# Performance work log

Measured on AMD Instinct MI355X. Metric: run time of the kernel, lower is better.

The kernel has to match this reference:

```python
import jax, jax.numpy as jnp
import numpy as np

B, C, H, W = 32, 512, 28, 28
NUM_CLASSES = 200
THRESHOLD = 0.6


def _conv(x, w, b, pad):
    y = jax.lax.conv_general_dilated(
        x, w, window_strides=(1, 1), padding=[(pad, pad), (pad, pad)],
        dimension_numbers=('NCHW', 'OIHW', 'NCHW'))
    return y + b[None, :, None, None]


def _classifier(x, w1, b1, w2, b2, w3, b3):
    x = jax.nn.relu(_conv(x, w1, b1, 1))
    x = jax.nn.relu(_conv(x, w2, b2, 1))
    return _conv(x, w3, b3, 0)


def _avg_pool3(x):
    # torch F.avg_pool2d(k=3, stride=1, pad=1, count_include_pad=True): sum window / 9
    s = jax.lax.reduce_window(x, 0.0, jax.lax.add, (1, 1, 3, 3), (1, 1, 1, 1),
                              [(0, 0), (0, 0), (1, 1), (1, 1)])
    return s / 9.0


def setup_inputs() -> dict:
    key = jax.random.key(0)
    ks = jax.random.split(key, 16)
    sc = 0.02
    inp = {
        'x': jax.random.normal(ks[0], (B, C, H, W), jnp.float32),
        'label': jax.random.randint(ks[1], (B, NUM_CLASSES), 0, 2),
        'w1a': jax.random.normal(ks[2], (1024, 512, 3, 3), jnp.float32) * sc,
        'b1a': jax.random.normal(ks[3], (1024,), jnp.float32) * sc,
        'w2a': jax.random.normal(ks[4], (1024, 1024, 3, 3), jnp.float32) * sc,
        'b2a': jax.random.normal(ks[5], (1024,), jnp.float32) * sc,
        'w3a': jax.random.normal(ks[6], (NUM_CLASSES, 1024, 1, 1), jnp.float32) * sc,
        'b3a': jax.random.normal(ks[7], (NUM_CLASSES,), jnp.float32) * sc,
        'w1b': jax.random.normal(ks[8], (1024, 512, 3, 3), jnp.float32) * sc,
        'b1b': jax.random.normal(ks[9], (1024,), jnp.float32) * sc,
        'w2b': jax.random.normal(ks[10], (1024, 1024, 3, 3), jnp.float32) * sc,
        'b2b': jax.random.normal(ks[11], (1024,), jnp.float32) * sc,
        'w3b': jax.random.normal(ks[12], (NUM_CLASSES, 1024, 1, 1), jnp.float32) * sc,
        'b3b': jax.random.normal(ks[13], (NUM_CLASSES,), jnp.float32) * sc,
    }
    return inp


def reference(x, label, w1a, b1a, w2a, b2a, w3a, b3a,
              w1b, b1b, w2b, b2b, w3b, b3b):
    feats = _avg_pool3(x)                       # [B,512,H,W]
    out_A = _classifier(feats, w1a, b1a, w2a, b2a, w3a, b3a)  # [B,K,H,W]
    logits_A = out_A.mean(axis=(2, 3))          # [B,K]

    # attention map: per-sample max over channels whose label is nonzero,
    # floored at 0 (the loop seeds the channel stack with a zeros map)
    sel = jnp.where(label[:, :, None, None] > 0, out_A, -jnp.inf)
    atten = jnp.maximum(sel.max(axis=1), 0.0)   # [B,H,W]

    # per-sample min-max normalization over HxW
    mins = atten.min(axis=(1, 2), keepdims=True)
    maxs = atten.max(axis=(1, 2), keepdims=True)
    atten_n = (atten - mins) / (maxs - mins)

    # threshold-erase mask (constant w.r.t. autograd, matching torch code)
    mask = jax.lax.stop_gradient(jnp.where(atten_n >= THRESHOLD, 0.0, 1.0))
    feats_erased = feats * mask[:, None, :, :]

    out_B = _classifier(feats_erased, w1b, b1b, w2b, b2b, w3b, b3b)
    logits_B = out_B.mean(axis=(2, 3))
    return logits_A, logits_B
```

## Files before the change

kernel.cpp:

```cpp
#include <hip/hip_runtime.h>
#include <hip/hip_bf16.h>

typedef unsigned long long ull;
typedef __attribute__((ext_vector_type(8))) short short8;
typedef __attribute__((ext_vector_type(8))) __bf16 bf16x8;
typedef __attribute__((ext_vector_type(4))) float floatx4;

#define GLL16(gp, lp) __builtin_amdgcn_global_load_lds( \
  (__attribute__((address_space(1))) void*)(gp), \
  (__attribute__((address_space(3))) void*)(lp), 16, 0, 0)

#define WVM(N) asm volatile("s_waitcnt vmcnt(" #N ")" ::: "memory")

__device__ __forceinline__ floatx4 mfma16(short8 a, short8 b, floatx4 c){
  return __builtin_amdgcn_mfma_f32_16x16x32_bf16(
      __builtin_bit_cast(bf16x8, a), __builtin_bit_cast(bf16x8, b), c, 0, 0, 0);
}

__device__ __forceinline__ unsigned pkbf(float a, float b){
  unsigned ua = __float_as_uint(a), ub = __float_as_uint(b);
  ua += 0x7fffu + ((ua >> 16) & 1u);
  ub += 0x7fffu + ((ub >> 16) & 1u);
  return (ua >> 16) | (ub & 0xffff0000u);
}

__global__ __launch_bounds__(256) void pool_kernel(const float* __restrict__ x,
                                                   unsigned short* __restrict__ out){
  __shared__ float xs[16*784];
  const int tid = threadIdx.x;
  const int b = blockIdx.x >> 5, cg = blockIdx.x & 31;
  const float* src = x + ((size_t)b*512 + cg*16)*784;
  for (int i=tid;i<16*784;i+=256) xs[i]=src[i];
  __syncthreads();
  unsigned* dst = (unsigned*)out + ((size_t)b*960)*256 + cg*8;
  for (int o=tid;o<30*32*8;o+=256){
    int cip = o & 7, pos = o >> 3;
    int row = pos >> 5, col = pos & 31;
    float s0=0.f, s1=0.f;
    if (row>=1 && row<=28 && col>=1 && col<=28){
      int h=row-1, w=col-1;
      const float* p0 = &xs[(cip*2)*784];
      const float* p1 = p0 + 784;
      #pragma unroll
      for (int dh=-1;dh<=1;++dh){ int hh=h+dh; if ((unsigned)hh<28u){
        #pragma unroll
        for (int dw=-1;dw<=1;++dw){ int ww=w+dw; if((unsigned)ww<28u){
          s0 += p0[hh*28+ww]; s1 += p1[hh*28+ww]; } } } }
      s0 /= 9.f; s1 /= 9.f;
    }
    dst[(size_t)pos*256 + cip] = pkbf(s0, s1);
  }
}

template<int CIN>
__global__ __launch_bounds__(256) void prep3x3(const float* __restrict__ w,
                                               unsigned short* __restrict__ Wt){
  __shared__ float wsm[CIN*9];
  const int co = blockIdx.x, tid = threadIdx.x;
  const float* src = w + (size_t)co*(CIN*9);
  for (int i=tid;i<CIN*9;i+=256) wsm[i]=src[i];
  __syncthreads();
  for (int o=tid;o<9*(CIN/2);o+=256){
    int t = o/(CIN/2), cp = o - t*(CIN/2);
    unsigned v = pkbf(wsm[(cp*2)*9+t], wsm[(cp*2+1)*9+t]);
    ((unsigned*)Wt)[(((size_t)t*1024+co)*CIN>>1) + cp] = v;
  }
}

__global__ __launch_bounds__(256) void prep1x1(const float* __restrict__ w3,
                                               unsigned short* __restrict__ Wp){
  const int row = blockIdx.x, tid = threadIdx.x;
  unsigned* dst = (unsigned*)Wp + (size_t)row*512;
  if (row < 200){
    const float* src = w3 + (size_t)row*1024;
    for (int j=tid;j<512;j+=256) dst[j] = pkbf(src[2*j], src[2*j+1]);
  } else {
    for (int j=tid;j<512;j+=256) dst[j] = 0u;
  }
}

template<int CIN>
__global__ __launch_bounds__(256, 2) void conv3x3_v10(
    const unsigned short* __restrict__ X,
    const unsigned short* __restrict__ Wt,
    const float* __restrict__ bias,
    unsigned short* __restrict__ Out)
{
  constexpr int NCH = CIN/32;
  constexpr size_t CB = (size_t)CIN*2;
  constexpr size_t TAPSTR = (size_t)1024*CB;
  __shared__ char Als[24576];
  __shared__ char Bls[20480];

  const int tid = threadIdx.x;
  const int l = tid & 63, wv = tid >> 6;
  const int cog = wv & 1, pg = wv >> 1;
  const int bid = blockIdx.x;
  const int co0 = (bid & 7) << 7;
  const int y = bid >> 3;
  const int b = y >> 2, rb = y & 3;
  const int r0 = rb << 3;
  const bool active = (pg == 0) || (rb < 3);

  const int sbyt = (l*16) ^ (((l>>3)&7)<<4);
  const int srow = sbyt >> 6;
  const int sw   = sbyt & 63;

  const ull aS0 = (ull)Wt + (size_t)(co0 + (wv*2)*16   + srow)*CB + sw;
  const ull aS1 = (ull)Wt + (size_t)(co0 + (wv*2+1)*16 + srow)*CB + sw;
  ull bS[5];
  #pragma unroll
  for (int k=0;k<5;++k){
    int q = (wv + 4*k)*16 + srow;
    int trow = q >> 5, tcol = q & 31;
    int ir = r0 + trow; if (ir > 29) ir = 29;
    bS[k] = (ull)X + ((size_t)b*960 + ir*32 + tcol)*CB + sw;
  }

  const int jl = l & 15, g = l >> 4;
  int paE[4];
  #pragma unroll
  for (int m=0;m<4;++m){
    int xo = (cog*64 + m*16 + jl)*64 + g*16;
    paE[m] = xo ^ (((xo>>7)&7)<<4);
  }
  int pbS[3][7];
  #pragma unroll
  for (int f=0;f<7;++f){
    int p = pg*112 + f*16 + jl;
    int hl = p/28, cl = p - hl*28;
    #pragma unroll
    for (int ss=0;ss<3;++ss){
      int xo = (hl*32 + cl + ss)*64 + g*16;
      pbS[ss][f] = xo ^ (((xo>>7)&7)<<4);
    }
  }

  floatx4 acc[4][7];
  #pragma unroll
  for (int m=0;m<4;++m)
    #pragma unroll
    for (int f=0;f<7;++f) acc[m][f] = (floatx4){0.f,0.f,0.f,0.f};

  #pragma unroll
  for (int k=0;k<5;++k) GLL16((const void*)bS[k], Bls + (wv + 4*k)*1024);
  GLL16((const void*)aS0,            Als +        (wv*2)*1024);
  GLL16((const void*)aS1,            Als +        (wv*2+1)*1024);
  GLL16((const void*)(aS0 + TAPSTR), Als + 8192 + (wv*2)*1024);
  GLL16((const void*)(aS1 + TAPSTR), Als + 8192 + (wv*2+1)*1024);

  #pragma unroll 1
  for (int c=0;c<NCH;++c){
    #pragma unroll
    for (int t=0;t<9;++t){
      const int rr = t/3, ss = t - rr*3;
      if (t == 0 && c > 0){
        #pragma unroll
        for (int k=0;k<5;++k)
          GLL16((const void*)(bS[k] + (size_t)c*64), Bls + (wv + 4*k)*1024);
      }
      {
        const int stTap = (t<7) ? t+2 : t-7;
        const size_t aoff = (size_t)stTap*TAPSTR + (size_t)(c + (t>=7))*64;
        const int sd = ((t+2)%3)*8192;
        GLL16((const void*)(aS0 + aoff), Als + sd + (wv*2)*1024);
        GLL16((const void*)(aS1 + aoff), Als + sd + (wv*2+1)*1024);
      }
      if (t == 0) { WVM(2); } else { WVM(4); }
      __builtin_amdgcn_s_barrier();
      if (active){
        const char* ap = Als + (t%3)*8192;
        short8 a0 = *(const short8*)(ap + paE[0]);
        short8 a1 = *(const short8*)(ap + paE[1]);
        short8 a2 = *(const short8*)(ap + paE[2]);
        short8 a3 = *(const short8*)(ap + paE[3]);
        short8 bv[7];
        #pragma unroll
        for (int f=0;f<7;++f)
          bv[f] = *(const short8*)(Bls + (pbS[ss][f] + rr*2048));
        __builtin_amdgcn_s_setprio(1);
        #pragma unroll
        for (int f=0;f<7;++f){
          acc[0][f] = mfma16(a0, bv[f], acc[0][f]);
          acc[1][f] = mfma16(a1, bv[f], acc[1][f]);
          acc[2][f] = mfma16(a2, bv[f], acc[2][f]);
          acc[3][f] = mfma16(a3, bv[f], acc[3][f]);
        }
        __builtin_amdgcn_s_setprio(0);
      }
      __builtin_amdgcn_s_barrier();
    }
  }

  if (!active) return;

  #pragma unroll
  for (int m=0;m<4;++m){
    const int coL = cog*64 + m*16 + g*4;
    const float4 bv4 = *(const float4*)&bias[co0 + coL];
    #pragma unroll
    for (int f=0;f<7;++f){
      int pp = pg*112 + f*16 + jl;
      int hl = pp/28, cl = pp - hl*28;
      float v0 = fmaxf(acc[m][f][0] + bv4.x, 0.f);
      float v1 = fmaxf(acc[m][f][1] + bv4.y, 0.f);
      float v2 = fmaxf(acc[m][f][2] + bv4.z, 0.f);
      float v3 = fmaxf(acc[m][f][3] + bv4.w, 0.f);
      uint2 pk; pk.x = pkbf(v0,v1); pk.y = pkbf(v2,v3);
      size_t oa = ((size_t)b*960 + (size_t)(r0 + hl + 1)*32 + (cl + 1))*1024 + (co0 + coL);
      *(uint2*)(Out + oa) = pk;
    }
  }
}

template<int CIN, bool K3, bool BF16OUT>
__global__ __launch_bounds__(512, 2) void conv_mfma(
    const unsigned short* __restrict__ X,
    const unsigned short* __restrict__ Wt,
    const float* __restrict__ bias, int biasN,
    void* __restrict__ Out)
{
  constexpr int T9 = K3 ? 9 : 1;
  constexpr int NA = K3 ? 9 : 1;
  __shared__ short Als[T9*4096];
  __shared__ short Bls[10240];
  __shared__ float biasLs[128];

  const int tid = threadIdx.x;
  const int l = tid & 63, wv = tid >> 6;
  const int wc = wv & 3, wp = wv >> 2;
  const int co0 = blockIdx.x << 7;
  const int by = blockIdx.y;
  const int b = by >> 2, rb = by & 3;
  const int r0 = rb << 3;
  const int nrh = (rb < 3) ? 10 : 6;
  const int NB = 2*nrh;
  const bool active = (wp == 0) || (rb < 3);

  if (tid < 128) biasLs[tid] = (co0 + tid < biasN) ? bias[co0 + tid] : 0.f;

  const size_t laneOff = (size_t)(l >> 2)*(CIN*2) + (size_t)(l & 3)*16;

  ull aB[NA];
  #pragma unroll
  for (int j=0;j<NA;++j){
    int k = wv*NA + j;
    int t = K3 ? (k >> 3) : 0;
    int cog2 = K3 ? (k & 7) : k;
    aB[j] = (ull)Wt + ((size_t)(t*1024 + co0 + cog2*16)*(CIN*2)) + laneOff;
  }
  const ull xBase = (ull)X + ((size_t)b*960)*(CIN*2) + (size_t)(r0*32)*(CIN*2) + laneOff;
  ull bB0=0, bB1=0, bB2=0; int nb=0;
  if (wv < NB)      { bB0 = xBase + (size_t)(wv*16)*(CIN*2);      nb = 1; }
  if (wv + 8 < NB)  { bB1 = xBase + (size_t)((wv+8)*16)*(CIN*2);  nb = 2; }
  if (wv + 16 < NB) { bB2 = xBase + (size_t)((wv+16)*16)*(CIN*2); nb = 3; }

  const int jl = l & 15, g = l >> 4;
  int paE[2];
  #pragma unroll
  for (int m=0;m<2;++m) paE[m] = (wc*32 + m*16 + jl)*32 + g*8;
  int pbE[7], ph[7], pc[7];
  #pragma unroll
  for (int f=0;f<7;++f){
    int p = wp*112 + f*16 + jl;
    int hl = p / 28, cl = p - hl*28;
    ph[f]=hl; pc[f]=cl;
    pbE[f] = (hl*32 + cl)*32 + g*8;
  }

  floatx4 acc[2][7];
  #pragma unroll
  for (int m=0;m<2;++m)
    #pragma unroll
    for (int f=0;f<7;++f) acc[m][f] = (floatx4){0.f,0.f,0.f,0.f};

  const int NCH = CIN/32;
  for (int c=0;c<NCH;++c){
    if (c) __syncthreads();
    const size_t cOff = (size_t)c*64;
    #pragma unroll
    for (int j=0;j<NA;++j)
      GLL16((const void*)(aB[j] + cOff), (char*)Als + (wv*NA + j)*1024);
    GLL16((const void*)(bB0 + cOff), (char*)Bls + wv*1024);
    if (nb > 1) GLL16((const void*)(bB1 + cOff), (char*)Bls + (wv+8)*1024);
    if (nb > 2) GLL16((const void*)(bB2 + cOff), (char*)Bls + (wv+16)*1024);
    __syncthreads();
    if (active){
      #pragma unroll
      for (int t=0;t<T9;++t){
        const int tA = t*4096;
        const int tB = K3 ? (((t/3)*32 + (t - (t/3)*3))*32) : ((1*32+1)*32);
        short8 a0 = *(const short8*)&Als[tA + paE[0]];
        short8 a1 = *(const short8*)&Als[tA + paE[1]];
        #pragma unroll
        for (int f=0;f<7;++f){
          short8 bvv = *(const short8*)&Bls[tB + pbE[f]];
          acc[0][f] = mfma16(a0, bvv, acc[0][f]);
          acc[1][f] = mfma16(a1, bvv, acc[1][f]);
        }
      }
    }
  }

  if (!active) return;

  #pragma unroll
  for (int m=0;m<2;++m){
    const int coL = wc*32 + m*16 + g*4;
    const float4 bv4 = *(const float4*)&biasLs[coL];
    #pragma unroll
    for (int f=0;f<7;++f){
      float v0 = acc[m][f][0] + bv4.x;
      float v1 = acc[m][f][1] + bv4.y;
      float v2 = acc[m][f][2] + bv4.z;
      float v3 = acc[m][f][3] + bv4.w;
      if constexpr (BF16OUT){
        v0=fmaxf(v0,0.f); v1=fmaxf(v1,0.f); v2=fmaxf(v2,0.f); v3=fmaxf(v3,0.f);
        uint2 pk; pk.x = pkbf(v0,v1); pk.y = pkbf(v2,v3);
        size_t oa = ((size_t)b*960 + (size_t)(r0 + ph[f] + 1)*32 + (pc[f]+1))*1024 + (co0 + coL);
        *(uint2*)((unsigned short*)Out + oa) = pk;
      } else {
        int co = co0 + coL;
        if (co < 200){
          int p = wp*112 + f*16 + jl;
          size_t oa = ((size_t)b*784 + (size_t)(r0*28) + p)*200 + co;
          float4 ov; ov.x=v0; ov.y=v1; ov.z=v2; ov.w=v3;
          *(float4*)((float*)Out + oa) = ov;
        }
      }
    }
  }
}

__global__ __launch_bounds__(256) void logits_kernel(const float* __restrict__ outC,
                                                     float* __restrict__ dst){
  const int b = blockIdx.x, seg = blockIdx.y;
  const int co = threadIdx.x;
  if (co >= 200) return;
  const float* base = outC + ((size_t)b*784 + seg*98)*200 + co;
  float s = 0.f;
  for (int p=0;p<98;++p) s += base[(size_t)p*200];
  atomicAdd(&dst[b*200+co], s*(1.f/784.f));
}

__global__ __launch_bounds__(256) void atten_kernel(const float* __restrict__ outC,
                                                    const int* __restrict__ label,
                                                    float* __restrict__ mask){
  __shared__ float al[784];
  __shared__ float redn[256], redx[256];
  __shared__ unsigned char lab[200];
  const int b = blockIdx.x, tid = threadIdx.x;
  for (int i=tid;i<200;i+=256) lab[i] = label[b*200+i] > 0 ? 1 : 0;
  __syncthreads();
  for (int p=tid;p<784;p+=256){
    const float* row = outC + ((size_t)b*784+p)*200;
    float m = -__builtin_inff();
    for (int c=0;c<200;++c) if (lab[c]) m = fmaxf(m, row[c]);
    al[p] = fmaxf(m, 0.f);
  }
  __syncthreads();
  float mn = __builtin_inff(), mx = -__builtin_inff();
  for (int p=tid;p<784;p+=256){ float v=al[p]; mn=fminf(mn,v); mx=fmaxf(mx,v); }
  redn[tid]=mn; redx[tid]=mx; __syncthreads();
  for (int s2=128;s2>0;s2>>=1){
    if (tid<s2){ redn[tid]=fminf(redn[tid],redn[tid+s2]); redx[tid]=fmaxf(redx[tid],redx[tid+s2]); }
    __syncthreads();
  }
  mn = redn[0]; mx = redx[0];
  for (int p=tid;p<784;p+=256){
    float nrm = (al[p]-mn)/(mx-mn);
    mask[b*784+p] = (nrm >= 0.6f) ? 0.f : 1.f;
  }
}

__global__ __launch_bounds__(256) void erase_kernel(const unsigned short* __restrict__ feats,
                                                    const float* __restrict__ mask,
                                                    unsigned short* __restrict__ dst){
  const int blk = blockIdx.x; const int b = blk/30, row = blk - b*30;
  const size_t base = ((size_t)b*960 + row*32)*512;
  for (int i=threadIdx.x; i<4096; i+=256){
    int col = i >> 7;
    float mv = 0.f;
    if (row>=1 && row<=28 && col>=1 && col<=28) mv = mask[b*784 + (row-1)*28 + (col-1)];
    uint2 v = make_uint2(0u,0u);
    if (mv > 0.5f) v = *(const uint2*)(feats + base + (size_t)i*4);
    *(uint2*)(dst + base + (size_t)i*4) = v;
  }
}

extern "C" void kernel_launch(void* const* d_in, const int* in_sizes, int n_in,
                              void* d_out, int out_size, void* d_ws, size_t ws_size,
                              hipStream_t stream){
  (void)in_sizes; (void)n_in; (void)out_size; (void)ws_size;
  const float* x   = (const float*)d_in[0];
  const int* label = (const int*)d_in[1];
  const float* w1a = (const float*)d_in[2];  const float* b1a = (const float*)d_in[3];
  const float* w2a = (const float*)d_in[4];  const float* b2a = (const float*)d_in[5];
  const float* w3a = (const float*)d_in[6];  const float* b3a = (const float*)d_in[7];
  const float* w1b = (const float*)d_in[8];  const float* b1b = (const float*)d_in[9];
  const float* w2b = (const float*)d_in[10]; const float* b2b = (const float*)d_in[11];
  const float* w3b = (const float*)d_in[12]; const float* b3b = (const float*)d_in[13];

  char* ws = (char*)d_ws;
  unsigned short* WtS = (unsigned short*)(ws);
  unsigned short* WtL = (unsigned short*)(ws + 9441280);
  unsigned short* W3p = (unsigned short*)(ws + 28319744);
  unsigned short* F   = (unsigned short*)(ws + 28848128);
  unsigned short* G1  = (unsigned short*)(ws + 60309504);
  unsigned short* G2  = (unsigned short*)(ws + 123228160);
  float* outC  = (float*)(ws + 186146816);
  float* maskB = (float*)(ws + 206217216);
  float* logA = (float*)d_out;
  float* logB = logA + 6400;

  hipMemsetAsync(G1, 0, 62914560, stream);
  hipMemsetAsync(G2, 0, 62914560, stream);
  hipMemsetAsync(d_out, 0, 51200, stream);

  pool_kernel<<<1024,256,0,stream>>>(x, F);

  prep3x3<512><<<1024,256,0,stream>>>(w1a, WtS);
  conv3x3_v10<512><<<1024,256,0,stream>>>(F, WtS, b1a, G1);
  prep3x3<1024><<<1024,256,0,stream>>>(w2a, WtL);
  conv3x3_v10<1024><<<1024,256,0,stream>>>(G1, WtL, b2a, G2);
  prep1x1<<<256,256,0,stream>>>(w3a, W3p);
  conv_mfma<1024,false,false><<<dim3(2,128),512,0,stream>>>(G2, W3p, b3a, 200, outC);
  logits_kernel<<<dim3(32,8),256,0,stream>>>(outC, logA);
  atten_kernel<<<32,256,0,stream>>>(outC, label, maskB);
  erase_kernel<<<960,256,0,stream>>>(F, maskB, G1);

  prep3x3<512><<<1024,256,0,stream>>>(w1b, WtS);
  conv3x3_v10<512><<<1024,256,0,stream>>>(G1, WtS, b1b, G2);
  prep3x3<1024><<<1024,256,0,stream>>>(w2b, WtL);
  conv3x3_v10<1024><<<1024,256,0,stream>>>(G2, WtL, b2b, G1);
  prep1x1<<<256,256,0,stream>>>(w3b, W3p);
  conv_mfma<1024,false,false><<<dim3(2,128),512,0,stream>>>(G1, W3p, b3b, 200, outC);
  logits_kernel<<<dim3(32,8),256,0,stream>>>(outC, logB);
}
```

Baseline: 1.487 ms.

## Retile 3x3 conv to 256 output channels per block with per-wave weight buffers

The 3x3 conv kernel now gives each block 256 output channels and 4 image rows (112 pixels), with every wave owning 64 channels. Each wave stages its own weight slices in private LDS buffers, so the per-tap block barriers are gone and only one barrier per input-channel chunk remains. Activation tiles are double-buffered and prefetched mid-chunk, and the idle-wave handling for the last row-band is removed. The intent is to cut synchronisation and wasted waves, at the cost of more LDS per block (72KB), which may limit occupancy, and a grid of 896 blocks.

```diff
diff --git a/kernel.cpp b/kernel.cpp
--- a/kernel.cpp
+++ b/kernel.cpp
@@ -80,7 +80,7 @@
 }
 
 template<int CIN>
-__global__ __launch_bounds__(256, 2) void conv3x3_v10(
+__global__ __launch_bounds__(256, 2) void conv3x3_v13(
     const unsigned short* __restrict__ X,
     const unsigned short* __restrict__ Wt,
     const float* __restrict__ bias,
@@ -89,45 +89,44 @@
   constexpr int NCH = CIN/32;
   constexpr size_t CB = (size_t)CIN*2;
   constexpr size_t TAPSTR = (size_t)1024*CB;
-  __shared__ char Als[24576];
-  __shared__ char Bls[20480];
+  __shared__ char Als[49152];
+  __shared__ char Bls[24576];
 
   const int tid = threadIdx.x;
   const int l = tid & 63, wv = tid >> 6;
-  const int cog = wv & 1, pg = wv >> 1;
   const int bid = blockIdx.x;
-  const int co0 = (bid & 7) << 7;
-  const int y = bid >> 3;
-  const int b = y >> 2, rb = y & 3;
-  const int r0 = rb << 3;
-  const bool active = (pg == 0) || (rb < 3);
+  const int co0 = (bid & 3) << 8;
+  const int y = bid >> 2;
+  const int b = y & 31, yt = y >> 5;
+  const int r0 = yt << 2;
 
   const int sbyt = (l*16) ^ (((l>>3)&7)<<4);
   const int srow = sbyt >> 6;
   const int sw   = sbyt & 63;
 
-  const ull aS0 = (ull)Wt + (size_t)(co0 + (wv*2)*16   + srow)*CB + sw;
-  const ull aS1 = (ull)Wt + (size_t)(co0 + (wv*2+1)*16 + srow)*CB + sw;
-  ull bS[5];
-  #pragma unroll
-  for (int k=0;k<5;++k){
+  ull aS[4];
+  #pragma unroll
+  for (int k=0;k<4;++k)
+    aS[k] = (ull)Wt + (size_t)(co0 + wv*64 + k*16 + srow)*CB + sw;
+  ull bS[3];
+  #pragma unroll
+  for (int k=0;k<3;++k){
     int q = (wv + 4*k)*16 + srow;
-    int trow = q >> 5, tcol = q & 31;
-    int ir = r0 + trow; if (ir > 29) ir = 29;
-    bS[k] = (ull)X + ((size_t)b*960 + ir*32 + tcol)*CB + sw;
+    int hr = q >> 5, col = q & 31;
+    bS[k] = (ull)X + ((size_t)b*960 + (r0 + hr)*32 + col)*CB + sw;
   }
 
   const int jl = l & 15, g = l >> 4;
   int paE[4];
   #pragma unroll
   for (int m=0;m<4;++m){
-    int xo = (cog*64 + m*16 + jl)*64 + g*16;
+    int xo = (m*16 + jl)*64 + g*16;
     paE[m] = xo ^ (((xo>>7)&7)<<4);
   }
   int pbS[3][7];
   #pragma unroll
   for (int f=0;f<7;++f){
-    int p = pg*112 + f*16 + jl;
+    int p = f*16 + jl;
     int hl = p/28, cl = p - hl*28;
     #pragma unroll
     for (int ss=0;ss<3;++ss){
@@ -142,34 +141,41 @@
     #pragma unroll
     for (int f=0;f<7;++f) acc[m][f] = (floatx4){0.f,0.f,0.f,0.f};
 
-  #pragma unroll
-  for (int k=0;k<5;++k) GLL16((const void*)bS[k], Bls + (wv + 4*k)*1024);
-  GLL16((const void*)aS0,            Als +        (wv*2)*1024);
-  GLL16((const void*)aS1,            Als +        (wv*2+1)*1024);
-  GLL16((const void*)(aS0 + TAPSTR), Als + 8192 + (wv*2)*1024);
-  GLL16((const void*)(aS1 + TAPSTR), Als + 8192 + (wv*2+1)*1024);
+  char* const myA = Als + wv*12288;
+
+  #pragma unroll
+  for (int k=0;k<3;++k) GLL16((const void*)bS[k], Bls + (wv + 4*k)*1024);
+  #pragma unroll
+  for (int k=0;k<4;++k) GLL16((const void*)aS[k],            myA +        k*1024);
+  #pragma unroll
+  for (int k=0;k<4;++k) GLL16((const void*)(aS[k] + TAPSTR), myA + 4096 + k*1024);
+  WVM(4);
+  __builtin_amdgcn_s_barrier();
 
   #pragma unroll 1
   for (int c=0;c<NCH;++c){
+    const bool lastc = (c == NCH-1);
+    const char* Bp = Bls + (c&1)*12288;
     #pragma unroll
     for (int t=0;t<9;++t){
       const int rr = t/3, ss = t - rr*3;
-      if (t == 0 && c > 0){
-        #pragma unroll
-        for (int k=0;k<5;++k)
-          GLL16((const void*)(bS[k] + (size_t)c*64), Bls + (wv + 4*k)*1024);
-      }
       {
         const int stTap = (t<7) ? t+2 : t-7;
         const size_t aoff = (size_t)stTap*TAPSTR + (size_t)(c + (t>=7))*64;
-        const int sd = ((t+2)%3)*8192;
-        GLL16((const void*)(aS0 + aoff), Als + sd + (wv*2)*1024);
-        GLL16((const void*)(aS1 + aoff), Als + sd + (wv*2+1)*1024);
+        char* sd = myA + ((t+2)%3)*4096;
+        #pragma unroll
+        for (int k=0;k<4;++k)
+          GLL16((const void*)(aS[k] + aoff), sd + k*1024);
       }
-      if (t == 0) { WVM(2); } else { WVM(4); }
-      __builtin_amdgcn_s_barrier();
-      if (active){
-        const char* ap = Als + (t%3)*8192;
+      if (t == 4 && !lastc){
+        #pragma unroll
+        for (int k=0;k<3;++k)
+          GLL16((const void*)(bS[k] + (size_t)(c+1)*64),
+                Bls + (((c+1)&1)*12288) + (wv + 4*k)*1024);
+      }
+      if ((t == 4 || t == 5) && !lastc) { WVM(11); } else { WVM(8); }
+      {
+        const char* ap = myA + (t%3)*4096;
         short8 a0 = *(const short8*)(ap + paE[0]);
         short8 a1 = *(const short8*)(ap + paE[1]);
         short8 a2 = *(const short8*)(ap + paE[2]);
@@ -177,7 +183,7 @@
         short8 bv[7];
         #pragma unroll
         for (int f=0;f<7;++f)
-          bv[f] = *(const short8*)(Bls + (pbS[ss][f] + rr*2048));
+          bv[f] = *(const short8*)(Bp + (pbS[ss][f] + rr*2048));
         __builtin_amdgcn_s_setprio(1);
         #pragma unroll
         for (int f=0;f<7;++f){
@@ -188,19 +194,17 @@
         }
         __builtin_amdgcn_s_setprio(0);
       }
-      __builtin_amdgcn_s_barrier();
-    }
-  }
-
-  if (!active) return;
+      if (t == 8) __builtin_amdgcn_s_barrier();
+    }
+  }
 
   #pragma unroll
   for (int m=0;m<4;++m){
-    const int coL = cog*64 + m*16 + g*4;
+    const int coL = wv*64 + m*16 + g*4;
     const float4 bv4 = *(const float4*)&bias[co0 + coL];
     #pragma unroll
     for (int f=0;f<7;++f){
-      int pp = pg*112 + f*16 + jl;
+      int pp = f*16 + jl;
       int hl = pp/28, cl = pp - hl*28;
       float v0 = fmaxf(acc[m][f][0] + bv4.x, 0.f);
       float v1 = fmaxf(acc[m][f][1] + bv4.y, 0.f);
@@ -420,9 +424,9 @@
   pool_kernel<<<1024,256,0,stream>>>(x, F);
 
   prep3x3<512><<<1024,256,0,stream>>>(w1a, WtS);
-  conv3x3_v10<512><<<1024,256,0,stream>>>(F, WtS, b1a, G1);
+  conv3x3_v13<512><<<896,256,0,stream>>>(F, WtS, b1a, G1);
   prep3x3<1024><<<1024,256,0,stream>>>(w2a, WtL);
-  conv3x3_v10<1024><<<1024,256,0,stream>>>(G1, WtL, b2a, G2);
+  conv3x3_v13<1024><<<896,256,0,stream>>>(G1, WtL, b2a, G2);
   prep1x1<<<256,256,0,stream>>>(w3a, W3p);
   conv_mfma<1024,false,false><<<dim3(2,128),512,0,stream>>>(G2, W3p, b3a, 200, outC);
   logits_kernel<<<dim3(32,8),256,0,stream>>>(outC, logA);
@@ -430,9 +434,9 @@
   erase_kernel<<<960,256,0,stream>>>(F, maskB, G1);
 
   prep3x3<512><<<1024,256,0,stream>>>(w1b, WtS);
-  conv3x3_v10<512><<<1024,256,0,stream>>>(G1, WtS, b1b, G2);
+  conv3x3_v13<512><<<896,256,0,stream>>>(G1, WtS, b1b, G2);
   prep3x3<1024><<<1024,256,0,stream>>>(w2b, WtL);
-  conv3x3_v10<1024><<<1024,256,0,stream>>>(G2, WtL, b2b, G1);
+  conv3x3_v13<1024><<<896,256,0,stream>>>(G2, WtL, b2b, G1);
   prep1x1<<<256,256,0,stream>>>(w3b, W3p);
   conv_mfma<1024,false,false><<<dim3(2,128),512,0,stream>>>(G1, W3p, b3b, 200, outC);
   logits_kernel<<<dim3(32,8),256,0,stream>>>(outC, logB);
```

New measurement: 1.529 ms. 1.03x slower.
